# Performance work log

Measured on AMD Instinct MI355X. Metric: run time of the kernel, lower is better.

The kernel has to match this reference:

```python
import jax, jax.numpy as jnp
import numpy as np

B, N, DIM, H = 8, 1024, 1024, 16
D = DIM // H  # head dim = 64
SCALE = DIM ** (-0.5)  # NOTE: original uses full dim, not head dim


def setup_inputs() -> dict:
    key = jax.random.key(0)
    ks = jax.random.split(key, 8)
    x = jax.random.normal(ks[0], (B, N, DIM), dtype=jnp.float32)
    pos = jax.random.normal(ks[1], (B, N, DIM), dtype=jnp.float32)
    mask = jax.random.bernoulli(ks[2], 0.9, (B, N - 1))  # bool, [b, n-1]
    w_std = 0.02
    W_qk = jax.random.normal(ks[3], (2 * DIM, DIM), dtype=jnp.float32) * w_std  # Linear(dim, 2*dim_qk)
    W_v = jax.random.normal(ks[4], (DIM, DIM), dtype=jnp.float32) * w_std
    W_out = jax.random.normal(ks[5], (DIM, DIM), dtype=jnp.float32) * w_std
    b_out = jax.random.normal(ks[6], (DIM,), dtype=jnp.float32) * w_std
    return {"x": x, "mask": mask, "pos": pos, "W_qk": W_qk, "W_v": W_v,
            "W_out": W_out, "b_out": b_out}


def _split_heads(t):
    # b n (h d) -> b h n d
    b, n, _ = t.shape
    return t.reshape(b, n, H, D).transpose(0, 2, 1, 3)


def reference(x, mask, pos, W_qk, W_v, W_out, b_out):
    qk = x @ W_qk.T                       # [b, n, 2*dim]
    q, k = jnp.split(qk, 2, axis=-1)
    v = x @ W_v.T                         # [b, n, dim]
    q, k, v = _split_heads(q), _split_heads(k), _split_heads(v)  # [b,h,n,d]
    hpos = _split_heads(pos)
    q = q + hpos
    k = k + hpos
    dots = jnp.einsum('bhid,bhjd->bhij', q, k) * SCALE  # [b,h,n,n]
    mask_value = -jnp.finfo(dots.dtype).max
    # pad mask with True at position 0 (CLS token always visible)
    m = jnp.pad(mask, ((0, 0), (1, 0)), constant_values=True)  # [b, n]
    m2 = m[:, None, :] & m[:, :, None]                          # [b, n, n]
    dots = jnp.where(m2[:, None, :, :], dots, mask_value)
    attn = jax.nn.softmax(dots, axis=-1)
    out = jnp.einsum('bhij,bhjd->bhid', attn, v)  # [b,h,n,d]
    out = out.transpose(0, 2, 1, 3).reshape(x.shape[0], x.shape[1], DIM)  # b n (h d)
    out = out @ W_out.T + b_out  # dropout p=0.0 -> identity
    return out
```

## Files before the change

### kernel.cpp

```cpp
#include <hip/hip_runtime.h>


typedef unsigned short u16;
typedef short bf16x8 __attribute__((ext_vector_type(8)));
typedef float f32x4 __attribute__((ext_vector_type(4)));
typedef float f32x16 __attribute__((ext_vector_type(16)));

#define MFMA16(a, b, c) __builtin_amdgcn_mfma_f32_16x16x32_bf16((a), (b), (c), 0, 0, 0)
#define MFMA32(a, b, c) __builtin_amdgcn_mfma_f32_32x32x16_bf16((a), (b), (c), 0, 0, 0)

__device__ __forceinline__ u16 f2bf(float f) {
    union { float f; unsigned u; } x; x.f = f;
    unsigned r = x.u + 0x7fffu + ((x.u >> 16) & 1u);
    return (u16)(r >> 16);
}

__device__ __forceinline__ void gld16(const u16* g, u16* l) {
    __builtin_amdgcn_global_load_lds(
        (const __attribute__((address_space(1))) void*)g,
        (__attribute__((address_space(3))) void*)l, 16, 0, 0);
}

__global__ __launch_bounds__(256) void cast_all(
    const float* __restrict__ x, const float* __restrict__ wqk,
    const float* __restrict__ wv, const float* __restrict__ wout,
    u16* __restrict__ xbf, u16* __restrict__ wqkvbf, u16* __restrict__ woutbf) {
    int i = blockIdx.x * 256 + threadIdx.x;
    const float* src; u16* dst; int off;
    if (i < 2097152)      { src = x;    dst = xbf;              off = i; }
    else if (i < 2621440) { src = wqk;  dst = wqkvbf;           off = i - 2097152; }
    else if (i < 2883584) { src = wv;   dst = wqkvbf + 2097152; off = i - 2621440; }
    else                  { src = wout; dst = woutbf;           off = i - 2883584; }
    float4 v = ((const float4*)src)[off];
    ushort4 o;
    o.x = f2bf(v.x); o.y = f2bf(v.y); o.z = f2bf(v.z); o.w = f2bf(v.w);
    ((ushort4*)dst)[off] = o;
}

#define GEMM_STAGE(c, k0_, PA, PB)                                                     \
    do {                                                                               \
        _Pragma("unroll")                                                              \
        for (int p = 0; p < 4; ++p) {                                                  \
            int rbase = w * 32 + p * 8;                                                \
            gld16((PA) + (size_t)(m0 + rbase + sr) * 1024 + (k0_) + scx,               \
                  &SS[c][0][rbase * 64]);                                              \
            gld16((PB) + (size_t)(n0 + rbase + sr) * 1024 + (k0_) + scx,               \
                  &SS[c][1][rbase * 64]);                                              \
        }                                                                              \
    } while (0)

__global__ __launch_bounds__(256) void gemm_qk(
    const u16* __restrict__ A,
    const u16* __restrict__ Bw,
    const float* __restrict__ pos,
    u16* __restrict__ Q, u16* __restrict__ Kx) {
    const int n0 = blockIdx.x * 128, m0 = blockIdx.y * 128;
    const int t = threadIdx.x, w = t >> 6, ln = t & 63;
    const int l15 = ln & 15, l4 = ln >> 4;
    const int wm = (w >> 1) * 64, wn = (w & 1) * 64;

    __shared__ u16 SS[2][2][128 * 64];

    f32x4 acc[4][4];
#pragma unroll
    for (int i = 0; i < 4; ++i)
#pragma unroll
        for (int j = 0; j < 4; ++j) acc[i][j] = (f32x4){0.f, 0.f, 0.f, 0.f};

    const int sr = ln >> 3;
    const int scx = ((ln & 7) ^ sr) * 8;
    const int x0 = (l15 & 7);

    GEMM_STAGE(0, 0, A, Bw);
    int cur = 0;
    for (int k0 = 0; k0 < 1024; k0 += 64) {
        if (k0 < 960) {
            GEMM_STAGE(cur ^ 1, k0 + 64, A, Bw);
            asm volatile("s_waitcnt vmcnt(8)" ::: "memory");
        } else {
            asm volatile("s_waitcnt vmcnt(0)" ::: "memory");
        }
        __builtin_amdgcn_s_barrier();
        const u16* Asb = SS[cur][0];
        const u16* Bsb = SS[cur][1];
#pragma unroll
        for (int kt = 0; kt < 2; ++kt) {
            bf16x8 a[4], bfr[4];
#pragma unroll
            for (int mt = 0; mt < 4; ++mt)
                a[mt] = *(const bf16x8*)&Asb[(wm + mt * 16 + l15) * 64 + ((kt * 4 + l4) ^ x0) * 8];
#pragma unroll
            for (int nt = 0; nt < 4; ++nt)
                bfr[nt] = *(const bf16x8*)&Bsb[(wn + nt * 16 + l15) * 64 + ((kt * 4 + l4) ^ x0) * 8];
#pragma unroll
            for (int mt = 0; mt < 4; ++mt)
#pragma unroll
                for (int nt = 0; nt < 4; ++nt)
                    acc[mt][nt] = MFMA16(a[mt], bfr[nt], acc[mt][nt]);
        }
        __builtin_amdgcn_sched_barrier(0);
        __builtin_amdgcn_s_barrier();
        cur ^= 1;
    }
#pragma unroll
    for (int mt = 0; mt < 4; ++mt)
#pragma unroll
        for (int nt = 0; nt < 4; ++nt)
#pragma unroll
            for (int r = 0; r < 4; ++r) {
                int i = m0 + wm + mt * 16 + l4 * 4 + r;
                int j = n0 + wn + nt * 16 + l15;
                int bb = i >> 10, n = i & 1023;
                int jj = j & 1023;
                float v = acc[mt][nt][r] + pos[(size_t)i * 1024 + jj];
                int hh = jj >> 6, dd = jj & 63;
                size_t idx = (((size_t)(bb * 16 + hh)) * 1024 + n) * 64 + dd;
                if (j < 1024) Q[idx] = f2bf(v * 0.045084220027780106f);
                else          Kx[idx] = f2bf(v);
            }
}

__global__ __launch_bounds__(256) void zero_k(
    const int* __restrict__ maskIn,
    u16* __restrict__ Kx) {
    int tid = blockIdx.x * 256 + threadIdx.x;
    int seg = tid & 7;
    int row = tid >> 3;
    int n = row & 1023;
    int b = row >> 14;
    if (n == 0) return;
    if (maskIn[b * 1023 + n - 1] != 0) return;
    uint4 z = {0u, 0u, 0u, 0u};
    *(uint4*)(Kx + (size_t)row * 64 + seg * 8) = z;
}

__global__ __launch_bounds__(256) void gemm_v(
    const u16* __restrict__ Wv,
    const u16* __restrict__ X,
    u16* __restrict__ Vt) {
    const int n0 = blockIdx.x * 128, m0 = blockIdx.y * 128;
    const int bIdx = blockIdx.z;
    const u16* Xb = X + (size_t)bIdx * 1048576;
    const int t = threadIdx.x, w = t >> 6, ln = t & 63;
    const int l15 = ln & 15, l4 = ln >> 4;
    const int wm = (w >> 1) * 64, wn = (w & 1) * 64;

    __shared__ u16 SS[2][2][128 * 64];

    f32x4 acc[4][4];
#pragma unroll
    for (int i = 0; i < 4; ++i)
#pragma unroll
        for (int j = 0; j < 4; ++j) acc[i][j] = (f32x4){0.f, 0.f, 0.f, 0.f};

    const int sr = ln >> 3;
    const int scx = ((ln & 7) ^ sr) * 8;
    const int x0 = (l15 & 7);

    GEMM_STAGE(0, 0, Wv, Xb);
    int cur = 0;
    for (int k0 = 0; k0 < 1024; k0 += 64) {
        if (k0 < 960) {
            GEMM_STAGE(cur ^ 1, k0 + 64, Wv, Xb);
            asm volatile("s_waitcnt vmcnt(8)" ::: "memory");
        } else {
            asm volatile("s_waitcnt vmcnt(0)" ::: "memory");
        }
        __builtin_amdgcn_s_barrier();
        const u16* Asb = SS[cur][0];
        const u16* Bsb = SS[cur][1];
#pragma unroll
        for (int kt = 0; kt < 2; ++kt) {
            bf16x8 a[4], bfr[4];
#pragma unroll
            for (int mt = 0; mt < 4; ++mt)
                a[mt] = *(const bf16x8*)&Asb[(wm + mt * 16 + l15) * 64 + ((kt * 4 + l4) ^ x0) * 8];
#pragma unroll
            for (int nt = 0; nt < 4; ++nt)
                bfr[nt] = *(const bf16x8*)&Bsb[(wn + nt * 16 + l15) * 64 + ((kt * 4 + l4) ^ x0) * 8];
#pragma unroll
            for (int mt = 0; mt < 4; ++mt)
#pragma unroll
                for (int nt = 0; nt < 4; ++nt)
                    acc[mt][nt] = MFMA16(a[mt], bfr[nt], acc[mt][nt]);
        }
        __builtin_amdgcn_sched_barrier(0);
        __builtin_amdgcn_s_barrier();
        cur ^= 1;
    }
#pragma unroll
    for (int mt = 0; mt < 4; ++mt)
#pragma unroll
        for (int nt = 0; nt < 4; ++nt)
#pragma unroll
            for (int r = 0; r < 4; ++r) {
                int i = m0 + wm + mt * 16 + l4 * 4 + r;
                int j = n0 + wn + nt * 16 + l15;
                Vt[((size_t)(bIdx * 1024 + i)) * 1024 + j] = f2bf(acc[mt][nt][r]);
            }
}

__global__ __launch_bounds__(64) void vsum_kernel(const u16* __restrict__ Vt,
                                                  const int* __restrict__ maskIn,
                                                  float* __restrict__ Vsum,
                                                  float* __restrict__ Vmask) {
    int row = blockIdx.x, ln = threadIdx.x;
    int b = row >> 10;
    const u16* p = Vt + (size_t)row * 1024 + ln * 16;
    uint4 a = *(const uint4*)p;
    uint4 bq = *(const uint4*)(p + 8);
    float s = 0.f, sm = 0.f;
    unsigned vv[8] = {a.x, a.y, a.z, a.w, bq.x, bq.y, bq.z, bq.w};
#pragma unroll
    for (int i = 0; i < 8; ++i) {
        int j0 = ln * 16 + 2 * i;
        float lo = __uint_as_float(vv[i] << 16);
        float hi = __uint_as_float(vv[i] & 0xffff0000u);
        s += lo + hi;
        bool ok0 = (j0 == 0) || (maskIn[b * 1023 + j0 - 1] != 0);
        bool ok1 = (maskIn[b * 1023 + j0] != 0);
        if (!ok0) sm += lo;
        if (!ok1) sm += hi;
    }
#pragma unroll
    for (int d = 1; d < 64; d <<= 1) { s += __shfl_xor(s, d); sm += __shfl_xor(sm, d); }
    if (ln == 0) { Vsum[row] = s; Vmask[row] = sm; }
}

__global__ __launch_bounds__(512) void attn_kernel(
    const u16* __restrict__ Q,
    const u16* __restrict__ Kx,
    const u16* __restrict__ Vt,
    const int* __restrict__ maskIn,
    const float* __restrict__ Vsum,
    const float* __restrict__ Vmask,
    u16* __restrict__ O) {
    const int gid = blockIdx.x;
    const int bh = gid & 127;
    const int qt = gid >> 7;
    const int b = bh >> 4, h = bh & 15;
    const int t = threadIdx.x, w = t >> 6, ln = t & 63;
    const int half = w >> 2, wq = w & 3;
    const int l31 = ln & 31, l5 = ln >> 5;

    __shared__ __align__(16) char lds[65568];
    float* nm = (float*)(lds + 65536);

    {
        float cnt = 0.f;
        for (int i = t; i < 1023; i += 512)
            cnt += (maskIn[b * 1023 + i] == 0) ? 1.f : 0.f;
#pragma unroll
        for (int d = 1; d < 64; d <<= 1) cnt += __shfl_xor(cnt, d);
        if (ln == 0) nm[w] = cnt;
    }

    const size_t qkbase = (size_t)bh * 65536;
    const int q0 = qt * 128 + wq * 32;
    const int q = q0 + l31;

    bf16x8 bq[4];
#pragma unroll
    for (int kt = 0; kt < 4; ++kt)
        bq[kt] = *(const bf16x8*)(Q + qkbase + (size_t)q * 64 + kt * 16 + l5 * 8);

    float lsum = 0.f;
    f32x16 o0 = {0,0,0,0,0,0,0,0,0,0,0,0,0,0,0,0};
    f32x16 o1 = {0,0,0,0,0,0,0,0,0,0,0,0,0,0,0,0};

    const int jbase = half * 512;
    const int srow = ln >> 3;
    const int swz8 = (ln & 7) ^ srow;
    u16* ldsH = (u16*)(lds + half * 32768);
    const int rb = wq * 16;

#define ATTN_STAGE(c, j0_)                                                              \
    do {                                                                                \
        gld16(Kx + qkbase + (size_t)((j0_) + rb + srow) * 64 + swz8 * 8,                \
              ldsH + (c) * 8192 + rb * 64);                                             \
        gld16(Kx + qkbase + (size_t)((j0_) + rb + 8 + srow) * 64 + swz8 * 8,            \
              ldsH + (c) * 8192 + (rb + 8) * 64);                                       \
        gld16(Vt + qkbase + (size_t)(rb + srow) * 1024 + (j0_) + swz8 * 8,              \
              ldsH + (c) * 8192 + 4096 + rb * 64);                                      \
        gld16(Vt + qkbase + (size_t)(rb + 8 + srow) * 1024 + (j0_) + swz8 * 8,          \
              ldsH + (c) * 8192 + 4096 + (rb + 8) * 64);                                \
    } while (0)

    ATTN_STAGE(0, jbase);
    int cur = 0;
    for (int jt = 0; jt < 8; ++jt) {
        const int j0 = jbase + jt * 64;
        if (jt < 7) {
            ATTN_STAGE(cur ^ 1, j0 + 64);
            asm volatile("s_waitcnt vmcnt(4)" ::: "memory");
        } else {
            asm volatile("s_waitcnt vmcnt(0)" ::: "memory");
        }
        __builtin_amdgcn_s_barrier();

        const u16* Kb = ldsH + cur * 8192;
        const u16* Vb = Kb + 4096;

        f32x16 st0 = {0,0,0,0,0,0,0,0,0,0,0,0,0,0,0,0};
        f32x16 st1 = {0,0,0,0,0,0,0,0,0,0,0,0,0,0,0,0};
        __builtin_amdgcn_s_setprio(1);
#pragma unroll
        for (int ktk = 0; ktk < 4; ++ktk) {
            const int sw = ((ktk * 2 + l5) ^ (l31 & 7)) * 8;
            bf16x8 ak0 = *(const bf16x8*)&Kb[l31 * 64 + sw];
            bf16x8 ak1 = *(const bf16x8*)&Kb[(32 + l31) * 64 + sw];
            st0 = MFMA32(ak0, bq[ktk], st0);
            st1 = MFMA32(ak1, bq[ktk], st1);
        }
        __builtin_amdgcn_s_setprio(0);
#pragma unroll
        for (int i = 0; i < 16; ++i) {
            float p0 = __builtin_amdgcn_exp2f(st0[i]);
            float p1 = __builtin_amdgcn_exp2f(st1[i]);
            st0[i] = p0;
            st1[i] = p1;
            lsum += p0 + p1;
        }
        unsigned pk0[8], pk1[8];
#pragma unroll
        for (int g = 0; g < 4; ++g) {
#pragma unroll
            for (int qq = 0; qq < 2; ++qq) {
                unsigned a0 = __float_as_uint(st0[g * 4 + 2 * qq]) + 0x8000u;
                unsigned a1 = __float_as_uint(st0[g * 4 + 2 * qq + 1]) + 0x8000u;
                pk0[2 * g + qq] = (a1 & 0xffff0000u) | (a0 >> 16);
                unsigned c0 = __float_as_uint(st1[g * 4 + 2 * qq]) + 0x8000u;
                unsigned c1 = __float_as_uint(st1[g * 4 + 2 * qq + 1]) + 0x8000u;
                pk1[2 * g + qq] = (c1 & 0xffff0000u) | (c0 >> 16);
            }
        }
        bf16x8 pf[4];
#pragma unroll
        for (int kt = 0; kt < 4; ++kt) {
            const int hh = kt & 1;
            unsigned own0, own1, off0, off1;
            if (kt < 2) {
                own0 = l5 ? pk0[4 * hh + 2] : pk0[4 * hh];
                own1 = l5 ? pk0[4 * hh + 3] : pk0[4 * hh + 1];
                off0 = l5 ? pk0[4 * hh]     : pk0[4 * hh + 2];
                off1 = l5 ? pk0[4 * hh + 1] : pk0[4 * hh + 3];
            } else {
                own0 = l5 ? pk1[4 * hh + 2] : pk1[4 * hh];
                own1 = l5 ? pk1[4 * hh + 3] : pk1[4 * hh + 1];
                off0 = l5 ? pk1[4 * hh]     : pk1[4 * hh + 2];
                off1 = l5 ? pk1[4 * hh + 1] : pk1[4 * hh + 3];
            }
            unsigned ex0 = (unsigned)__shfl_xor((int)off0, 32);
            unsigned ex1 = (unsigned)__shfl_xor((int)off1, 32);
            unsigned dw0 = l5 ? ex0 : own0;
            unsigned dw1 = l5 ? ex1 : own1;
            unsigned dw2 = l5 ? own0 : ex0;
            unsigned dw3 = l5 ? own1 : ex1;
            union { unsigned u[4]; bf16x8 v; } cv;
            cv.u[0] = dw0; cv.u[1] = dw1; cv.u[2] = dw2; cv.u[3] = dw3;
            pf[kt] = cv.v;
        }
        __builtin_amdgcn_s_setprio(1);
#pragma unroll
        for (int kt = 0; kt < 4; ++kt) {
            const int sw = ((kt * 2 + l5) ^ (l31 & 7)) * 8;
            bf16x8 av0 = *(const bf16x8*)&Vb[l31 * 64 + sw];
            bf16x8 av1 = *(const bf16x8*)&Vb[(32 + l31) * 64 + sw];
            o0 = MFMA32(av0, pf[kt], o0);
            o1 = MFMA32(av1, pf[kt], o1);
        }
        __builtin_amdgcn_s_setprio(0);
        __builtin_amdgcn_sched_barrier(0);
        __builtin_amdgcn_s_barrier();
        cur ^= 1;
    }
#undef ATTN_STAGE

    float* comb = (float*)lds;
    if (half == 1) {
        float* dst = comb + ((size_t)(wq * 64 + ln)) * 33;
#pragma unroll
        for (int i = 0; i < 16; ++i) { dst[i] = o0[i]; dst[16 + i] = o1[i]; }
        dst[32] = lsum;
    }
    __syncthreads();
    if (half == 0) {
        const float* src = comb + ((size_t)(wq * 64 + ln)) * 33;
#pragma unroll
        for (int i = 0; i < 16; ++i) { o0[i] += src[i]; o1[i] += src[16 + i]; }
        lsum += src[32];
        float lrow = lsum + __shfl_xor(lsum, 32);
        float nmaskb = nm[0] + nm[1] + nm[2] + nm[3] + nm[4] + nm[5] + nm[6] + nm[7];
        lrow -= nmaskb;
        const float linv = 1.f / lrow;
        const int n = q0 + l31;
        const bool rqv = (n == 0) || (maskIn[b * 1023 + n - 1] != 0);
        u16* orow = O + ((size_t)(b * 1024 + n)) * 1024 + h * 64;
#pragma unroll
        for (int g = 0; g < 4; ++g) {
            ushort4 s0, s1;
            unsigned short* p0 = (unsigned short*)&s0;
            unsigned short* p1 = (unsigned short*)&s1;
#pragma unroll
            for (int r = 0; r < 4; ++r) {
                int reg = 4 * g + r;
                int d0 = 8 * g + 4 * l5 + r;
                float v0 = rqv ? (o0[reg] - Vmask[bh * 64 + d0]) * linv
                               : Vsum[bh * 64 + d0] * 0.0009765625f;
                float v1 = rqv ? (o1[reg] - Vmask[bh * 64 + 32 + d0]) * linv
                               : Vsum[bh * 64 + 32 + d0] * 0.0009765625f;
                p0[r] = f2bf(v0);
                p1[r] = f2bf(v1);
            }
            *(ushort4*)&orow[8 * g + 4 * l5] = s0;
            *(ushort4*)&orow[32 + 8 * g + 4 * l5] = s1;
        }
    }
}

__global__ __launch_bounds__(256) void gemm_out(
    const u16* __restrict__ A,
    const u16* __restrict__ Bw,
    const float* __restrict__ bias,
    float* __restrict__ out) {
    const int n0 = blockIdx.x * 128, m0 = blockIdx.y * 128;
    const int t = threadIdx.x, w = t >> 6, ln = t & 63;
    const int l15 = ln & 15, l4 = ln >> 4;
    const int wm = (w >> 1) * 64, wn = (w & 1) * 64;

    __shared__ u16 SS[2][2][128 * 64];

    f32x4 acc[4][4];
#pragma unroll
    for (int i = 0; i < 4; ++i)
#pragma unroll
        for (int j = 0; j < 4; ++j) acc[i][j] = (f32x4){0.f, 0.f, 0.f, 0.f};

    const int sr = ln >> 3;
    const int scx = ((ln & 7) ^ sr) * 8;
    const int x0 = (l15 & 7);

    GEMM_STAGE(0, 0, A, Bw);
    int cur = 0;
    for (int k0 = 0; k0 < 1024; k0 += 64) {
        if (k0 < 960) {
            GEMM_STAGE(cur ^ 1, k0 + 64, A, Bw);
            asm volatile("s_waitcnt vmcnt(8)" ::: "memory");
        } else {
            asm volatile("s_waitcnt vmcnt(0)" ::: "memory");
        }
        __builtin_amdgcn_s_barrier();
        const u16* Asb = SS[cur][0];
        const u16* Bsb = SS[cur][1];
#pragma unroll
        for (int kt = 0; kt < 2; ++kt) {
            bf16x8 a[4], bfr[4];
#pragma unroll
            for (int mt = 0; mt < 4; ++mt)
                a[mt] = *(const bf16x8*)&Asb[(wm + mt * 16 + l15) * 64 + ((kt * 4 + l4) ^ x0) * 8];
#pragma unroll
            for (int nt = 0; nt < 4; ++nt)
                bfr[nt] = *(const bf16x8*)&Bsb[(wn + nt * 16 + l15) * 64 + ((kt * 4 + l4) ^ x0) * 8];
#pragma unroll
            for (int mt = 0; mt < 4; ++mt)
#pragma unroll
                for (int nt = 0; nt < 4; ++nt)
                    acc[mt][nt] = MFMA16(a[mt], bfr[nt], acc[mt][nt]);
        }
        __builtin_amdgcn_sched_barrier(0);
        __builtin_amdgcn_s_barrier();
        cur ^= 1;
    }
#pragma unroll
    for (int mt = 0; mt < 4; ++mt)
#pragma unroll
        for (int nt = 0; nt < 4; ++nt)
#pragma unroll
            for (int r = 0; r < 4; ++r) {
                int i = m0 + wm + mt * 16 + l4 * 4 + r;
                int j = n0 + wn + nt * 16 + l15;
                out[(size_t)i * 1024 + j] = acc[mt][nt][r] + bias[j];
            }
}

extern "C" void kernel_launch(void* const* d_in, const int* in_sizes, int n_in,
                              void* d_out, int out_size, void* d_ws, size_t ws_size,
                              hipStream_t stream) {
    const float* x    = (const float*)d_in[0];
    const int*   mask = (const int*)d_in[1];
    const float* pos  = (const float*)d_in[2];
    const float* wqk  = (const float*)d_in[3];
    const float* wv   = (const float*)d_in[4];
    const float* wout = (const float*)d_in[5];
    const float* bout = (const float*)d_in[6];

    char* ws = (char*)d_ws;
    u16* xbf    = (u16*)(ws + 0);
    u16* wqkvbf = (u16*)(ws + 16777216);
    u16* woutbf = (u16*)(ws + 23068672);
    u16* Qb     = (u16*)(ws + 25165824);
    u16* Kb     = (u16*)(ws + 41943040);
    u16* Vtb    = (u16*)(ws + 58720256);
    float* Vsum = (float*)(ws + 16777216);
    float* Vmask = (float*)(ws + 16777216 + 32768);

    cast_all<<<12288, 256, 0, stream>>>(x, wqk, wv, wout, xbf, wqkvbf, woutbf);

    gemm_qk<<<dim3(16, 64), 256, 0, stream>>>(xbf, wqkvbf, pos, Qb, Kb);
    zero_k<<<4096, 256, 0, stream>>>(mask, Kb);
    gemm_v<<<dim3(8, 8, 8), 256, 0, stream>>>(wqkvbf + 2097152, xbf, Vtb);
    vsum_kernel<<<8192, 64, 0, stream>>>(Vtb, mask, Vsum, Vmask);
    attn_kernel<<<1024, 512, 0, stream>>>(Qb, Kb, Vtb, mask, Vsum, Vmask, xbf);
    gemm_out<<<dim3(8, 64), 256, 0, stream>>>(xbf, woutbf, bout, (float*)d_out);
}
```

Baseline: 290.6 us.

## Replace direct-to-LDS loads with register-staged prefetch into padded LDS tiles

The attention kernel no longer issues global_load_lds with XOR-swizzled addressing. K and V tiles are now loaded into registers two iterations ahead and written to LDS after the PV MFMAs, using a 72-element padded row stride instead of the swizzle. This keeps one tile in flight in registers while computing on the current tile. It costs extra VGPRs and explicit LDS stores, and it replaces the vmcnt-based waits with full __syncthreads.

```diff
diff --git a/kernel.cpp b/kernel.cpp
--- a/kernel.cpp
+++ b/kernel.cpp
@@ -243,8 +243,9 @@
     const int half = w >> 2, wq = w & 3;
     const int l31 = ln & 31, l5 = ln >> 5;
 
-    __shared__ __align__(16) char lds[65568];
-    float* nm = (float*)(lds + 65536);
+    __shared__ __align__(16) char lds[73760];
+    float* nm = (float*)(lds + 73728);
+    u16* KsBase = (u16*)(lds + half * 36864);
 
     {
         float cnt = 0.f;
@@ -268,47 +269,45 @@
     f32x16 o0 = {0,0,0,0,0,0,0,0,0,0,0,0,0,0,0,0};
     f32x16 o1 = {0,0,0,0,0,0,0,0,0,0,0,0,0,0,0,0};
 
+    const int th = t & 255;
+    const int srow = th >> 2, sc = (th & 3) * 16;
     const int jbase = half * 512;
-    const int srow = ln >> 3;
-    const int swz8 = (ln & 7) ^ srow;
-    u16* ldsH = (u16*)(lds + half * 32768);
-    const int rb = wq * 16;
-
-#define ATTN_STAGE(c, j0_)                                                              \
+
+    uint4 kv, kv2, vv, vv2;
+#define ALOAD(j0_)                                                                      \
     do {                                                                                \
-        gld16(Kx + qkbase + (size_t)((j0_) + rb + srow) * 64 + swz8 * 8,                \
-              ldsH + (c) * 8192 + rb * 64);                                             \
-        gld16(Kx + qkbase + (size_t)((j0_) + rb + 8 + srow) * 64 + swz8 * 8,            \
-              ldsH + (c) * 8192 + (rb + 8) * 64);                                       \
-        gld16(Vt + qkbase + (size_t)(rb + srow) * 1024 + (j0_) + swz8 * 8,              \
-              ldsH + (c) * 8192 + 4096 + rb * 64);                                      \
-        gld16(Vt + qkbase + (size_t)(rb + 8 + srow) * 1024 + (j0_) + swz8 * 8,          \
-              ldsH + (c) * 8192 + 4096 + (rb + 8) * 64);                                \
+        kv  = *(const uint4*)(Kx + qkbase + (size_t)((j0_) + srow) * 64 + sc);          \
+        kv2 = *(const uint4*)(Kx + qkbase + (size_t)((j0_) + srow) * 64 + sc + 8);      \
+        vv  = *(const uint4*)(Vt + qkbase + (size_t)srow * 1024 + (j0_) + sc);          \
+        vv2 = *(const uint4*)(Vt + qkbase + (size_t)srow * 1024 + (j0_) + sc + 8);      \
     } while (0)
-
-    ATTN_STAGE(0, jbase);
+#define AWRITE(c)                                                                       \
+    do {                                                                                \
+        u16* Ksw = KsBase + (c) * 9216;                                                 \
+        u16* Vsw = Ksw + 4608;                                                          \
+        *(uint4*)&Ksw[srow * 72 + sc] = kv;                                             \
+        *(uint4*)&Ksw[srow * 72 + sc + 8] = kv2;                                        \
+        *(uint4*)&Vsw[srow * 72 + sc] = vv;                                             \
+        *(uint4*)&Vsw[srow * 72 + sc + 8] = vv2;                                        \
+    } while (0)
+
+    ALOAD(jbase);
+    AWRITE(0);
+    ALOAD(jbase + 64);
+    __syncthreads();
+
     int cur = 0;
     for (int jt = 0; jt < 8; ++jt) {
-        const int j0 = jbase + jt * 64;
-        if (jt < 7) {
-            ATTN_STAGE(cur ^ 1, j0 + 64);
-            asm volatile("s_waitcnt vmcnt(4)" ::: "memory");
-        } else {
-            asm volatile("s_waitcnt vmcnt(0)" ::: "memory");
-        }
-        __builtin_amdgcn_s_barrier();
-
-        const u16* Kb = ldsH + cur * 8192;
-        const u16* Vb = Kb + 4096;
+        const u16* Ks = KsBase + cur * 9216;
+        const u16* Vs = Ks + 4608;
 
         f32x16 st0 = {0,0,0,0,0,0,0,0,0,0,0,0,0,0,0,0};
         f32x16 st1 = {0,0,0,0,0,0,0,0,0,0,0,0,0,0,0,0};
         __builtin_amdgcn_s_setprio(1);
 #pragma unroll
         for (int ktk = 0; ktk < 4; ++ktk) {
-            const int sw = ((ktk * 2 + l5) ^ (l31 & 7)) * 8;
-            bf16x8 ak0 = *(const bf16x8*)&Kb[l31 * 64 + sw];
-            bf16x8 ak1 = *(const bf16x8*)&Kb[(32 + l31) * 64 + sw];
+            bf16x8 ak0 = *(const bf16x8*)&Ks[(l31) * 72 + ktk * 16 + l5 * 8];
+            bf16x8 ak1 = *(const bf16x8*)&Ks[(32 + l31) * 72 + ktk * 16 + l5 * 8];
             st0 = MFMA32(ak0, bq[ktk], st0);
             st1 = MFMA32(ak1, bq[ktk], st1);
         }
@@ -363,18 +362,23 @@
         __builtin_amdgcn_s_setprio(1);
 #pragma unroll
         for (int kt = 0; kt < 4; ++kt) {
-            const int sw = ((kt * 2 + l5) ^ (l31 & 7)) * 8;
-            bf16x8 av0 = *(const bf16x8*)&Vb[l31 * 64 + sw];
-            bf16x8 av1 = *(const bf16x8*)&Vb[(32 + l31) * 64 + sw];
+            bf16x8 av0 = *(const bf16x8*)&Vs[(l31) * 72 + kt * 16 + l5 * 8];
+            bf16x8 av1 = *(const bf16x8*)&Vs[(32 + l31) * 72 + kt * 16 + l5 * 8];
             o0 = MFMA32(av0, pf[kt], o0);
             o1 = MFMA32(av1, pf[kt], o1);
         }
         __builtin_amdgcn_s_setprio(0);
+
+        if (jt < 7) {
+            AWRITE(cur ^ 1);
+            if (jt < 6) ALOAD(jbase + (jt + 2) * 64);
+        }
         __builtin_amdgcn_sched_barrier(0);
-        __builtin_amdgcn_s_barrier();
+        __syncthreads();
         cur ^= 1;
     }
-#undef ATTN_STAGE
+#undef ALOAD
+#undef AWRITE
 
     float* comb = (float*)lds;
     if (half == 1) {
```

After: 285.2 us. Within noise of the previous version (-1.9%).
